# Kernel optimization log

Hardware: AMD Instinct MI355X
Metric: run time of the kernel (lower is better)

The kernel has to match this reference:

```python
import jax, jax.numpy as jnp
import numpy as np

B, J = 1000000, 17

def setup_inputs() -> dict:
    key = jax.random.key(0)
    k1, k2, k3 = jax.random.split(key, 3)
    output = jax.random.uniform(k1, (B, J, 3), dtype=jnp.float32)  # class channel in (0,1) for BCE
    reg_gt = jax.random.uniform(k2, (B, J, 2), dtype=jnp.float32)
    class_gt = (jax.random.uniform(k3, (B, J)) > 0.5).astype(jnp.float32)  # binary {0,1}
    target = jnp.concatenate([reg_gt, class_gt[:, :, None]], axis=2)
    return {"output": output, "target": target}

def reference(output, target):
    reg_pred = output[:, :, :2]          # [B,J,2]
    class_pred = output[:, :, 2]         # [B,J]
    reg_gt = target[:, :, :2]
    class_gt = target[:, :, 2]

    # nn.BCELoss (mean reduction), with torch's log clamp at -100
    log_p = jnp.maximum(jnp.log(class_pred), -100.0)
    log_1mp = jnp.maximum(jnp.log1p(-class_pred), -100.0)
    loss_class = -jnp.mean(class_gt * log_p + (1.0 - class_gt) * log_1mp)

    # masked_fill(mask < 0.5, 0) on BOTH pred and gt -> masked entries contribute 0 to MSE sum
    keep = class_pred[:, :, None] >= 0.5                       # [B,J,1] broadcast over 2 coords
    diff = jnp.where(keep, reg_pred - reg_gt, 0.0)             # [B,J,2]
    sq_sum = jnp.sum(diff * diff, axis=(1, 2))                 # [B]

    # per-batch joint count: 1 + #(class_gt == 1)
    num_joints = 1.0 + jnp.sum((class_gt == 1.0).astype(diff.dtype), axis=1)  # [B]

    loss_reg = jnp.mean(0.5 * sq_sum / num_joints)  # == (sum over batch)/batch_size
    return loss_class + loss_reg
```

## Files before the change

kernel.cpp:

```cpp
#include <hip/hip_runtime.h>
#include <hip/hip_bf16.h>

#define J_JOINTS 17
#define ROW_F 51
#define BLOCK 256
#define TILE_ROWS 128
#define TILE_F (TILE_ROWS * ROW_F)
#define GRID 768

__global__ __launch_bounds__(BLOCK) void loss_main_kernel(
    const float* __restrict__ outp,
    const float* __restrict__ tgt,
    double* __restrict__ acc,
    int B)
{
    __shared__ float so[TILE_F];
    __shared__ float st[TILE_F];

    const int tid  = threadIdx.x;
    const int r2   = tid >> 1;
    const int half = tid & 1;

    float cls_acc = 0.0f;
    float reg_acc = 0.0f;

    const int stride_rows = (int)gridDim.x * TILE_ROWS;

    for (int row0 = (int)blockIdx.x * TILE_ROWS; row0 < B; row0 += stride_rows) {
        const int rows_valid = min(TILE_ROWS, B - row0);
        const int nv = rows_valid * ROW_F;
        const int n4 = nv >> 2;

        const float4* src_o = reinterpret_cast<const float4*>(outp + row0 * ROW_F);
        const float4* src_t = reinterpret_cast<const float4*>(tgt  + row0 * ROW_F);
        float4* dst_o = reinterpret_cast<float4*>(so);
        float4* dst_t = reinterpret_cast<float4*>(st);
        for (int i = tid; i < n4; i += BLOCK) {
            dst_o[i] = src_o[i];
            dst_t[i] = src_t[i];
        }
        const int tb = n4 << 2;
        if (tid < (nv - tb)) {
            so[tb + tid] = outp[row0 * ROW_F + tb + tid];
            st[tb + tid] = tgt [row0 * ROW_F + tb + tid];
        }
        __syncthreads();

        float sq = 0.0f;
        float nj = 0.0f;
        if (r2 < rows_valid) {
            const int base = r2 * ROW_F + half * 24;
            #pragma unroll
            for (int k = 0; k < 8; ++k) {
                const float ox = so[base + 3*k + 0];
                const float oy = so[base + 3*k + 1];
                const float oz = so[base + 3*k + 2];
                const float tx = st[base + 3*k + 0];
                const float ty = st[base + 3*k + 1];
                const float tz = st[base + 3*k + 2];

                const bool gt1 = (tz == 1.0f);
                cls_acc += fmaxf(__logf(gt1 ? oz : (1.0f - oz)), -100.0f);

                const bool keep = (oz >= 0.5f);
                const float d0 = keep ? (ox - tx) : 0.0f;
                const float d1 = keep ? (oy - ty) : 0.0f;
                sq = fmaf(d0, d0, fmaf(d1, d1, sq));
                nj += gt1 ? 1.0f : 0.0f;
            }
            if (half) {
                const int b16 = r2 * ROW_F + 48;
                const float ox = so[b16 + 0];
                const float oy = so[b16 + 1];
                const float oz = so[b16 + 2];
                const float tx = st[b16 + 0];
                const float ty = st[b16 + 1];
                const float tz = st[b16 + 2];

                const bool gt1 = (tz == 1.0f);
                cls_acc += fmaxf(__logf(gt1 ? oz : (1.0f - oz)), -100.0f);

                const bool keep = (oz >= 0.5f);
                const float d0 = keep ? (ox - tx) : 0.0f;
                const float d1 = keep ? (oy - ty) : 0.0f;
                sq = fmaf(d0, d0, fmaf(d1, d1, sq));
                nj += gt1 ? 1.0f : 0.0f;
            }
        }

        sq += __shfl_xor(sq, 1, 64);
        nj += __shfl_xor(nj, 1, 64);
        if (!half && r2 < rows_valid) {
            reg_acc += __fdividef(0.5f * sq, 1.0f + nj);
        }
        __syncthreads();
    }

    #pragma unroll
    for (int m = 1; m < 64; m <<= 1) {
        cls_acc += __shfl_xor(cls_acc, m, 64);
        reg_acc += __shfl_xor(reg_acc, m, 64);
    }
    __shared__ float s_cls[BLOCK / 64];
    __shared__ float s_reg[BLOCK / 64];
    const int wid = tid >> 6;
    if ((tid & 63) == 0) {
        s_cls[wid] = cls_acc;
        s_reg[wid] = reg_acc;
    }
    __syncthreads();
    if (tid == 0) {
        float c = 0.0f, r = 0.0f;
        #pragma unroll
        for (int w = 0; w < BLOCK / 64; ++w) { c += s_cls[w]; r += s_reg[w]; }
        atomicAdd(&acc[0], (double)c);
        atomicAdd(&acc[1], (double)r);
    }
}

__global__ void loss_finalize_kernel(const double* __restrict__ acc,
                                     float* __restrict__ out, int B)
{
    const double cls_sum = acc[0];
    const double reg_sum = acc[1];
    const double loss_class = -cls_sum / ((double)B * (double)J_JOINTS);
    const double loss_reg   = reg_sum / (double)B;
    out[0] = (float)(loss_class + loss_reg);
}

extern "C" void kernel_launch(void* const* d_in, const int* in_sizes, int n_in,
                              void* d_out, int out_size, void* d_ws, size_t ws_size,
                              hipStream_t stream) {
    const float* outp = (const float*)d_in[0];
    const float* tgt  = (const float*)d_in[1];
    float* out = (float*)d_out;
    const int B = in_sizes[0] / (J_JOINTS * 3);

    double* acc = (double*)d_ws;
    hipMemsetAsync(acc, 0, 2 * sizeof(double), stream);

    loss_main_kernel<<<GRID, BLOCK, 0, stream>>>(outp, tgt, acc, B);
    loss_finalize_kernel<<<1, 1, 0, stream>>>(acc, out, B);
}
```

Before: 97.20 us.

## Double-buffer tiles with async global-to-LDS loads and four threads per row

Replaces the synchronous float4 global-to-shared copy with direct global_load_lds transfers into a double-buffered shared tile, so the next tile's load runs while the current tile is computed. The tile is halved to 64 rows to keep double-buffered LDS in budget, and each row is now split across four threads instead of two, with an extra shuffle step for the per-row reduction. This is meant to hide memory latency in a bandwidth-bound reduction, at the cost of more loop iterations, a vmcnt(0) wait each iteration, and use of a low-level builtin whose per-lane LDS addressing must match what the hardware expects.

Measured after the change: 87.49 us. -10.0%, faster.

```diff
diff --git a/kernel.cpp b/kernel.cpp
--- a/kernel.cpp
+++ b/kernel.cpp
@@ -1,12 +1,21 @@
 #include <hip/hip_runtime.h>
 #include <hip/hip_bf16.h>
+#include <stdint.h>
 
 #define J_JOINTS 17
 #define ROW_F 51
 #define BLOCK 256
-#define TILE_ROWS 128
+#define TILE_ROWS 64
 #define TILE_F (TILE_ROWS * ROW_F)
+#define TILE_CHUNKS (TILE_F / 4)
 #define GRID 768
+
+__device__ __forceinline__ void gld_lds16(const float* g, float* l) {
+    __builtin_amdgcn_global_load_lds(
+        (const __attribute__((address_space(1))) void*)g,
+        (__attribute__((address_space(3))) void*)l,
+        16, 0, 0);
+}
 
 __global__ __launch_bounds__(BLOCK) void loss_main_kernel(
     const float* __restrict__ outp,
@@ -14,50 +23,78 @@
     double* __restrict__ acc,
     int B)
 {
-    __shared__ float so[TILE_F];
-    __shared__ float st[TILE_F];
+    __shared__ float so[2][TILE_F];
+    __shared__ float st[2][TILE_F];
 
-    const int tid  = threadIdx.x;
-    const int r2   = tid >> 1;
-    const int half = tid & 1;
+    const int tid = threadIdx.x;
+    const int r4  = tid >> 2;
+    const int q   = tid & 3;
 
     float cls_acc = 0.0f;
     float reg_acc = 0.0f;
 
-    const int stride_rows = (int)gridDim.x * TILE_ROWS;
+    const int tiles_total = (B + TILE_ROWS - 1) / TILE_ROWS;
 
-    for (int row0 = (int)blockIdx.x * TILE_ROWS; row0 < B; row0 += stride_rows) {
-        const int rows_valid = min(TILE_ROWS, B - row0);
+    auto stage_async = [&](int row0, int buf) {
+        const float* go = outp + row0 * ROW_F;
+        const float* gt = tgt  + row0 * ROW_F;
+        float* lo = so[buf];
+        float* lt = st[buf];
+        #pragma unroll
+        for (int j = 0; j < 4; ++j) {
+            const int i = tid + j * BLOCK;
+            if (i < TILE_CHUNKS) {
+                gld_lds16(go + i * 4, lo + i * 4);
+                gld_lds16(gt + i * 4, lt + i * 4);
+            }
+        }
+    };
+    auto stage_sync = [&](int row0, int rows_valid, int buf) {
+        const float* go = outp + row0 * ROW_F;
+        const float* gt = tgt  + row0 * ROW_F;
         const int nv = rows_valid * ROW_F;
         const int n4 = nv >> 2;
-
-        const float4* src_o = reinterpret_cast<const float4*>(outp + row0 * ROW_F);
-        const float4* src_t = reinterpret_cast<const float4*>(tgt  + row0 * ROW_F);
-        float4* dst_o = reinterpret_cast<float4*>(so);
-        float4* dst_t = reinterpret_cast<float4*>(st);
         for (int i = tid; i < n4; i += BLOCK) {
-            dst_o[i] = src_o[i];
-            dst_t[i] = src_t[i];
+            reinterpret_cast<float4*>(so[buf])[i] = reinterpret_cast<const float4*>(go)[i];
+            reinterpret_cast<float4*>(st[buf])[i] = reinterpret_cast<const float4*>(gt)[i];
         }
         const int tb = n4 << 2;
-        if (tid < (nv - tb)) {
-            so[tb + tid] = outp[row0 * ROW_F + tb + tid];
-            st[tb + tid] = tgt [row0 * ROW_F + tb + tid];
+        if (tid < nv - tb) {
+            so[buf][tb + tid] = go[tb + tid];
+            st[buf][tb + tid] = gt[tb + tid];
         }
-        __syncthreads();
+    };
+    auto stage = [&](int tk, int buf) {
+        const int row0 = tk * TILE_ROWS;
+        if (row0 + TILE_ROWS <= B) stage_async(row0, buf);
+        else                       stage_sync(row0, B - row0, buf);
+    };
 
+    int tk  = blockIdx.x;
+    int cur = 0;
+
+    if (tk < tiles_total) stage(tk, 0);
+    asm volatile("s_waitcnt vmcnt(0)" ::: "memory");
+    __syncthreads();
+
+    while (tk < tiles_total) {
+        const int tn = tk + GRID;
+        if (tn < tiles_total) stage(tn, cur ^ 1);
+
+        const int rows_valid = min(TILE_ROWS, B - tk * TILE_ROWS);
         float sq = 0.0f;
         float nj = 0.0f;
-        if (r2 < rows_valid) {
-            const int base = r2 * ROW_F + half * 24;
+        if (r4 < rows_valid) {
+            const float* lo = so[cur] + r4 * ROW_F + q * 12;
+            const float* lt = st[cur] + r4 * ROW_F + q * 12;
             #pragma unroll
-            for (int k = 0; k < 8; ++k) {
-                const float ox = so[base + 3*k + 0];
-                const float oy = so[base + 3*k + 1];
-                const float oz = so[base + 3*k + 2];
-                const float tx = st[base + 3*k + 0];
-                const float ty = st[base + 3*k + 1];
-                const float tz = st[base + 3*k + 2];
+            for (int k = 0; k < 4; ++k) {
+                const float ox = lo[3*k + 0];
+                const float oy = lo[3*k + 1];
+                const float oz = lo[3*k + 2];
+                const float tx = lt[3*k + 0];
+                const float ty = lt[3*k + 1];
+                const float tz = lt[3*k + 2];
 
                 const bool gt1 = (tz == 1.0f);
                 cls_acc += fmaxf(__logf(gt1 ? oz : (1.0f - oz)), -100.0f);
@@ -68,14 +105,13 @@
                 sq = fmaf(d0, d0, fmaf(d1, d1, sq));
                 nj += gt1 ? 1.0f : 0.0f;
             }
-            if (half) {
-                const int b16 = r2 * ROW_F + 48;
-                const float ox = so[b16 + 0];
-                const float oy = so[b16 + 1];
-                const float oz = so[b16 + 2];
-                const float tx = st[b16 + 0];
-                const float ty = st[b16 + 1];
-                const float tz = st[b16 + 2];
+            if (q == 3) {
+                const float ox = lo[12 + 0];
+                const float oy = lo[12 + 1];
+                const float oz = lo[12 + 2];
+                const float tx = lt[12 + 0];
+                const float ty = lt[12 + 1];
+                const float tz = lt[12 + 2];
 
                 const bool gt1 = (tz == 1.0f);
                 cls_acc += fmaxf(__logf(gt1 ? oz : (1.0f - oz)), -100.0f);
@@ -87,13 +123,16 @@
                 nj += gt1 ? 1.0f : 0.0f;
             }
         }
-
-        sq += __shfl_xor(sq, 1, 64);
-        nj += __shfl_xor(nj, 1, 64);
-        if (!half && r2 < rows_valid) {
+        sq += __shfl_xor(sq, 1, 64);  nj += __shfl_xor(nj, 1, 64);
+        sq += __shfl_xor(sq, 2, 64);  nj += __shfl_xor(nj, 2, 64);
+        if (q == 0 && r4 < rows_valid) {
             reg_acc += __fdividef(0.5f * sq, 1.0f + nj);
         }
+
+        asm volatile("s_waitcnt vmcnt(0)" ::: "memory");
         __syncthreads();
+        cur ^= 1;
+        tk = tn;
     }
 
     #pragma unroll
```

## Replace LDS tile staging with per-thread vectorized register loads of 4-row groups

Applied to the files above, without the earlier changes.

Removes the shared-memory staging loop and syncthreads, and has each thread load four whole rows (51 float4) directly from global memory into registers and compute per-row sums. The persistent fixed grid is replaced by one thread per 4-row group, with a scalar tail path for leftover rows. This aims to cut LDS traffic and barrier overhead. In exchange, lanes read with a large stride and the kernel uses more registers.

Result: slower. 176.2 us (+81.2%).

```diff
diff --git a/kernel.cpp b/kernel.cpp
--- a/kernel.cpp
+++ b/kernel.cpp
@@ -4,96 +4,87 @@
 #define J_JOINTS 17
 #define ROW_F 51
 #define BLOCK 256
-#define TILE_ROWS 128
-#define TILE_F (TILE_ROWS * ROW_F)
-#define GRID 768
 
-__global__ __launch_bounds__(BLOCK) void loss_main_kernel(
+
+__global__ __launch_bounds__(BLOCK, 4) void loss_main_kernel(
     const float* __restrict__ outp,
     const float* __restrict__ tgt,
     double* __restrict__ acc,
     int B)
 {
-    __shared__ float so[TILE_F];
-    __shared__ float st[TILE_F];
-
-    const int tid  = threadIdx.x;
-    const int r2   = tid >> 1;
-    const int half = tid & 1;
+    const int tid = threadIdx.x;
+    const int g   = blockIdx.x * BLOCK + tid;
+    const int ngroups = B >> 2;
 
     float cls_acc = 0.0f;
     float reg_acc = 0.0f;
 
-    const int stride_rows = (int)gridDim.x * TILE_ROWS;
+    if (g < ngroups) {
+        const float4* O = reinterpret_cast<const float4*>(outp) + g * ROW_F;
+        const float4* T = reinterpret_cast<const float4*>(tgt)  + g * ROW_F;
 
-    for (int row0 = (int)blockIdx.x * TILE_ROWS; row0 < B; row0 += stride_rows) {
-        const int rows_valid = min(TILE_ROWS, B - row0);
-        const int nv = rows_valid * ROW_F;
-        const int n4 = nv >> 2;
+        float sq[4] = {0.f, 0.f, 0.f, 0.f};
+        float nj[4] = {0.f, 0.f, 0.f, 0.f};
 
-        const float4* src_o = reinterpret_cast<const float4*>(outp + row0 * ROW_F);
-        const float4* src_t = reinterpret_cast<const float4*>(tgt  + row0 * ROW_F);
-        float4* dst_o = reinterpret_cast<float4*>(so);
-        float4* dst_t = reinterpret_cast<float4*>(st);
-        for (int i = tid; i < n4; i += BLOCK) {
-            dst_o[i] = src_o[i];
-            dst_t[i] = src_t[i];
-        }
-        const int tb = n4 << 2;
-        if (tid < (nv - tb)) {
-            so[tb + tid] = outp[row0 * ROW_F + tb + tid];
-            st[tb + tid] = tgt [row0 * ROW_F + tb + tid];
-        }
-        __syncthreads();
+        #pragma unroll
+        for (int u = 0; u < 17; ++u) {
+            const float4 a0 = O[3*u + 0];
+            const float4 a1 = O[3*u + 1];
+            const float4 a2 = O[3*u + 2];
+            const float4 b0 = T[3*u + 0];
+            const float4 b1 = T[3*u + 1];
+            const float4 b2 = T[3*u + 2];
 
-        float sq = 0.0f;
-        float nj = 0.0f;
-        if (r2 < rows_valid) {
-            const int base = r2 * ROW_F + half * 24;
+            const float ox[4] = {a0.x, a0.w, a1.z, a2.y};
+            const float oy[4] = {a0.y, a1.x, a1.w, a2.z};
+            const float oz[4] = {a0.z, a1.y, a2.x, a2.w};
+            const float tx[4] = {b0.x, b0.w, b1.z, b2.y};
+            const float ty[4] = {b0.y, b1.x, b1.w, b2.z};
+            const float tz[4] = {b0.z, b1.y, b2.x, b2.w};
+
             #pragma unroll
-            for (int k = 0; k < 8; ++k) {
-                const float ox = so[base + 3*k + 0];
-                const float oy = so[base + 3*k + 1];
-                const float oz = so[base + 3*k + 2];
-                const float tx = st[base + 3*k + 0];
-                const float ty = st[base + 3*k + 1];
-                const float tz = st[base + 3*k + 2];
+            for (int jj = 0; jj < 4; ++jj) {
+                const int joint = 4*u + jj;
+                const int r = joint / 17;
 
-                const bool gt1 = (tz == 1.0f);
-                cls_acc += fmaxf(__logf(gt1 ? oz : (1.0f - oz)), -100.0f);
+                const bool gt1 = (tz[jj] == 1.0f);
+                cls_acc += fmaxf(__logf(gt1 ? oz[jj] : (1.0f - oz[jj])), -100.0f);
 
-                const bool keep = (oz >= 0.5f);
-                const float d0 = keep ? (ox - tx) : 0.0f;
-                const float d1 = keep ? (oy - ty) : 0.0f;
-                sq = fmaf(d0, d0, fmaf(d1, d1, sq));
-                nj += gt1 ? 1.0f : 0.0f;
-            }
-            if (half) {
-                const int b16 = r2 * ROW_F + 48;
-                const float ox = so[b16 + 0];
-                const float oy = so[b16 + 1];
-                const float oz = so[b16 + 2];
-                const float tx = st[b16 + 0];
-                const float ty = st[b16 + 1];
-                const float tz = st[b16 + 2];
-
-                const bool gt1 = (tz == 1.0f);
-                cls_acc += fmaxf(__logf(gt1 ? oz : (1.0f - oz)), -100.0f);
-
-                const bool keep = (oz >= 0.5f);
-                const float d0 = keep ? (ox - tx) : 0.0f;
-                const float d1 = keep ? (oy - ty) : 0.0f;
-                sq = fmaf(d0, d0, fmaf(d1, d1, sq));
-                nj += gt1 ? 1.0f : 0.0f;
+                const bool keep = (oz[jj] >= 0.5f);
+                const float d0 = keep ? (ox[jj] - tx[jj]) : 0.0f;
+                const float d1 = keep ? (oy[jj] - ty[jj]) : 0.0f;
+                sq[r] = fmaf(d0, d0, fmaf(d1, d1, sq[r]));
+                nj[r] += gt1 ? 1.0f : 0.0f;
             }
         }
 
-        sq += __shfl_xor(sq, 1, 64);
-        nj += __shfl_xor(nj, 1, 64);
-        if (!half && r2 < rows_valid) {
-            reg_acc += __fdividef(0.5f * sq, 1.0f + nj);
+        #pragma unroll
+        for (int r = 0; r < 4; ++r) {
+            reg_acc += __fdividef(0.5f * sq[r], 1.0f + nj[r]);
         }
-        __syncthreads();
+    }
+
+    const int tail0 = ngroups << 2;
+    if (blockIdx.x == 0 && tid < (B - tail0)) {
+        const int b = tail0 + tid;
+        float sq = 0.f, nj = 0.f;
+        for (int j = 0; j < J_JOINTS; ++j) {
+            const int base = b * ROW_F + 3*j;
+            const float ox = outp[base + 0];
+            const float oy = outp[base + 1];
+            const float oz = outp[base + 2];
+            const float tx = tgt[base + 0];
+            const float ty = tgt[base + 1];
+            const float tz = tgt[base + 2];
+            const bool gt1 = (tz == 1.0f);
+            cls_acc += fmaxf(__logf(gt1 ? oz : (1.0f - oz)), -100.0f);
+            const bool keep = (oz >= 0.5f);
+            const float d0 = keep ? (ox - tx) : 0.0f;
+            const float d1 = keep ? (oy - ty) : 0.0f;
+            sq = fmaf(d0, d0, fmaf(d1, d1, sq));
+            nj += gt1 ? 1.0f : 0.0f;
+        }
+        reg_acc += __fdividef(0.5f * sq, 1.0f + nj);
     }
 
     #pragma unroll
@@ -139,6 +130,8 @@
     double* acc = (double*)d_ws;
     hipMemsetAsync(acc, 0, 2 * sizeof(double), stream);
 
-    loss_main_kernel<<<GRID, BLOCK, 0, stream>>>(outp, tgt, acc, B);
+    const int ngroups = B >> 2;
+    const int blocks = (ngroups + BLOCK - 1) / BLOCK;
+    loss_main_kernel<<<blocks, BLOCK, 0, stream>>>(outp, tgt, acc, B);
     loss_finalize_kernel<<<1, 1, 0, stream>>>(acc, out, B);
 }
```
